# Performance work log

Hardware: AMD Instinct MI355X
Metric: run time of the kernel (lower is better)

The kernel has to match this reference:

```python
import jax, jax.numpy as jnp
import numpy as np

D, L, C, H, W = 4, 16, 64, 128, 128


def setup_inputs() -> dict:
    key = jax.random.key(0)
    ks = jax.random.split(key, 20)
    rn = lambda k, shape, s=0.02: jax.random.normal(k, shape, dtype=jnp.float32) * s
    return {
        "x": jax.random.normal(ks[0], (L, C, H, W), dtype=jnp.float32),
        "ln1_g": jnp.ones((D, C, H, W), jnp.float32),
        "ln1_b": jnp.zeros((D, C, H, W), jnp.float32),
        "Wq": rn(ks[1], (D, C, C)), "bq": jnp.zeros((D, C), jnp.float32),
        "Wk": rn(ks[2], (D, C, C)), "bk": jnp.zeros((D, C), jnp.float32),
        "Wv": rn(ks[3], (D, C, C)), "bv": jnp.zeros((D, C), jnp.float32),
        "Wa": rn(ks[4], (D, 1, 2 * C, 5, 5)), "ba": jnp.zeros((D, 1), jnp.float32),
        "ln2_g": jnp.ones((D, C, H, W), jnp.float32),
        "ln2_b": jnp.zeros((D, C, H, W), jnp.float32),
        "W1": rn(ks[5], (D, 2 * C, C)), "b1": jnp.zeros((D, 2 * C), jnp.float32),
        "W2": rn(ks[6], (D, C, 2 * C)), "b2": jnp.zeros((D, C), jnp.float32),
    }


def _layernorm(x, g, b):
    # torch nn.LayerNorm([C,H,W]): normalize over last 3 dims per frame, eps=1e-5
    mu = jnp.mean(x, axis=(1, 2, 3), keepdims=True)
    var = jnp.var(x, axis=(1, 2, 3), keepdims=True)
    return (x - mu) * jax.lax.rsqrt(var + 1e-5) * g[None] + b[None]


def _conv5(x, w):
    # x: [L, Cin, H, W], w: [1, Cin, 5, 5] -> [L, 1, H, W], SAME padding (pad=2)
    return jax.lax.conv_general_dilated(
        x, w, window_strides=(1, 1), padding="SAME",
        dimension_numbers=("NCHW", "OIHW", "NCHW"))


def _conv1x1(x, w, b):
    # 1x1 conv == per-pixel linear over channels
    return jnp.einsum("lchw,oc->lohw", x, w) + b[None, :, None, None]


def reference(x, ln1_g, ln1_b, Wq, bq, Wk, bk, Wv, bv, Wa, ba,
              ln2_g, ln2_b, W1, b1, W2, b2):
    depth = ln1_g.shape[0]
    c = Wa.shape[2] // 2
    for d in range(depth):
        # --- pre-norm conv attention (nheads=1) + residual ---
        h = _layernorm(x, ln1_g[d], ln1_b[d])
        Q = _conv1x1(h, Wq[d], bq[d])
        K = _conv1x1(h, Wk[d], bk[d])
        V = _conv1x1(h, Wv[d], bv[d])
        # conv_atten(cat([Q_i, K_j])) is linear in channels: split the 5x5
        # kernel into Q-part and K-part, so H_ij = A_i + B_j + bias.
        A = _conv5(Q, Wa[d, :, :c])[:, 0]   # [L, H, W]
        B = _conv5(K, Wa[d, :, c:])[:, 0]   # [L, H, W]
        S = A[:, None] + B[None, :] + ba[d][0]      # [L, L, H, W]
        P = jax.nn.softmax(S, axis=1)               # softmax over source frames j
        attn = jnp.einsum("ijhw,jchw->ichw", P, V)  # weighted sum of V_j
        x = x + attn
        # --- pre-norm conv FFN + residual ---
        h = _layernorm(x, ln2_g[d], ln2_b[d])
        f = _conv1x1(h, W1[d], b1[d])
        f = jax.nn.leaky_relu(f, 0.01)  # torch LeakyReLU default slope
        f = _conv1x1(f, W2[d], b2[d])
        x = x + f
    return x
```

## Files before the change

kernel.cpp:

```cpp
#include <hip/hip_runtime.h>


#define HW 16384
#define CHW 1048576
#define NB 64

typedef unsigned short u16;
typedef __attribute__((ext_vector_type(8))) short bf16x8;
typedef __attribute__((ext_vector_type(8))) unsigned short u16x8;
typedef __attribute__((ext_vector_type(4))) float f32x4;

static __device__ __forceinline__ u16 f2bf(float f) {
  union { float f; unsigned int u; } v; v.f = f;
  unsigned int r = v.u + 0x7fffu + ((v.u >> 16) & 1u);
  return (u16)(r >> 16);
}
static __device__ __forceinline__ float bf2f(u16 h) {
  union { unsigned int u; float f; } v; v.u = ((unsigned int)h) << 16;
  return v.f;
}
static __device__ __forceinline__ void ln_from_acc_wave(
    const float* acc, int l, int lane, float& mu, float& r) {
  const float invN = 1.f / 1048576.f;
  float2 v = *(const float2*)(acc + lane * 32 + 2 * l);
  float s = v.x, q = v.y;
#pragma unroll
  for (int off = 32; off > 0; off >>= 1) {
    s += __shfl_xor(s, off);
    q += __shfl_xor(q, off);
  }
  mu = s * invN;
  r = rsqrtf(q * invN - mu * mu + 1e-5f);
}

__global__ __launch_bounds__(256) void prep_kernel(
    const float* __restrict__ Wa, const float* __restrict__ Wk,
    const float* __restrict__ Wv, const float* __restrict__ W1,
    const float* __restrict__ W2, u16* __restrict__ w1pk,
    u16* __restrict__ w2pk, u16* __restrict__ wvpk, u16* __restrict__ wepk) {
  int d = blockIdx.x;
  int t = blockIdx.y * 256 + threadIdx.x;
  const int STR = 256 * 16;
  const float* WaK = Wa + ((size_t)d * 128 + 64) * 25;
  const float* Wkd = Wk + d * 4096;
  for (int idx = t; idx < 2048; idx += STR) {
    int frag = idx >> 9, lane = (idx >> 3) & 63, j = idx & 7;
    int mt = frag >> 1, kt = frag & 1;
    int tap = mt * 16 + (lane & 15);
    int ci = kt * 32 + (lane >> 4) * 8 + j;
    float s = 0.f;
    if (tap < 25)
      for (int co = 0; co < 64; ++co)
        s = fmaf(WaK[co * 25 + tap], Wkd[co * 64 + ci], s);
    wepk[d * 2048 + idx] = f2bf(s);
  }
  const float* Wvd = Wv + d * 4096;
  for (int idx = t; idx < 4096; idx += STR) {
    int frag = idx >> 9, lane = (idx >> 3) & 63, j = idx & 7;
    int mt = frag >> 1, kt = frag & 1;
    int co = mt * 16 + (lane & 15);
    int ci = kt * 32 + (lane >> 4) * 8 + j;
    wvpk[d * 4096 + idx] = f2bf(Wvd[co * 64 + ci]);
  }
  const float* W1d = W1 + d * 8192;
  for (int idx = t; idx < 8192; idx += STR) {
    int frag = idx >> 9, lane = (idx >> 3) & 63, j = idx & 7;
    int mt = frag >> 1, kt = frag & 1;
    int o = mt * 16 + (lane & 15);
    int ci = kt * 32 + (lane >> 4) * 8 + j;
    w1pk[d * 8192 + idx] = f2bf(W1d[o * 64 + ci]);
  }
  const float* W2d = W2 + d * 8192;
  for (int idx = t; idx < 8192; idx += STR) {
    int frag = idx >> 9, lane = (idx >> 3) & 63, j = idx & 7;
    int mt2 = frag >> 2, kt2 = frag & 3;
    int c = mt2 * 16 + (lane & 15);
    int o = kt2 * 32 + (lane >> 4) * 8 + j;
    w2pk[d * 8192 + idx] = f2bf(W2d[c * 128 + o]);
  }
}

__global__ __launch_bounds__(256) void lngb_kernel(
    const float* __restrict__ g1, const float* __restrict__ b1,
    const float* __restrict__ g2, const float* __restrict__ b2,
    u16* __restrict__ o1, u16* __restrict__ o2, u16* __restrict__ o3,
    u16* __restrict__ o4) {
  int idx = blockIdx.x * 256 + threadIdx.x;
  const float* src;
  u16* dst;
  switch (blockIdx.y) {
    case 0: src = g1; dst = o1; break;
    case 1: src = b1; dst = o2; break;
    case 2: src = g2; dst = o3; break;
    default: src = b2; dst = o4; break;
  }
  float4 v = *(const float4*)(src + (size_t)idx * 4);
  ushort4 o;
  o.x = f2bf(v.x); o.y = f2bf(v.y); o.z = f2bf(v.z); o.w = f2bf(v.w);
  *(ushort4*)(dst + (size_t)idx * 4) = o;
}

__global__ __launch_bounds__(256) void stats_kernel(
    const float* __restrict__ xin, float* __restrict__ acc) {
  int tid = threadIdx.x;
  size_t base = (size_t)blockIdx.x * 4096;
  const float4* in4 = (const float4*)(xin + base);
  float s = 0.f, q = 0.f;
#pragma unroll
  for (int k = 0; k < 4; ++k) {
    float4 v = in4[k * 256 + tid];
    s += v.x + v.y + v.z + v.w;
    q = fmaf(v.x, v.x, q); q = fmaf(v.y, v.y, q);
    q = fmaf(v.z, v.z, q); q = fmaf(v.w, v.w, q);
  }
#pragma unroll
  for (int off = 32; off > 0; off >>= 1) {
    s += __shfl_down(s, off); q += __shfl_down(q, off);
  }
  __shared__ float ls[4], lq[4];
  int wave = tid >> 6;
  if ((tid & 63) == 0) { ls[wave] = s; lq[wave] = q; }
  __syncthreads();
  if (tid == 0) {
    int frame = blockIdx.x >> 8;
    int bkt = blockIdx.x & (NB - 1);
    atomicAdd(&acc[bkt * 32 + frame * 2], ls[0] + ls[1] + ls[2] + ls[3]);
    atomicAdd(&acc[bkt * 32 + frame * 2 + 1], lq[0] + lq[1] + lq[2] + lq[3]);
  }
}

__global__ __launch_bounds__(256) void tb_kernel(
    const float* __restrict__ x, const u16* __restrict__ g,
    const u16* __restrict__ bln, const u16* __restrict__ wep_g,
    const float* __restrict__ accA, float* __restrict__ accBz,
    float* __restrict__ mulr, u16* __restrict__ T) {
  __shared__ __align__(16) char lds[18432];
  u16* hb = (u16*)lds;
  int tid = threadIdx.x;
  int l = blockIdx.y;
  int p0 = blockIdx.x << 7;
  if (blockIdx.x == 0 && blockIdx.y == 0)
    for (int i = tid; i < NB * 32; i += 256) accBz[i] = 0.f;
  int lane = tid & 63;
  float mu, r;
  ln_from_acc_wave(accA, l, lane, mu, r);
  if (blockIdx.x == 0 && tid == 0) {
    mulr[2 * l] = mu;
    mulr[2 * l + 1] = r;
  }

#pragma unroll
  for (int it = 0; it < 2; ++it) {
    int pq = tid & 31, cg = (tid >> 5) + it * 8;
    int px = pq * 4, c0 = cg * 4;
    float vv[4][4];
#pragma unroll
    for (int i = 0; i < 4; ++i) {
      int c = c0 + i;
      size_t gi = (((size_t)l * 64 + c) << 14) + p0 + px;
      int li = (c << 14) + p0 + px;
      float4 xv = *(const float4*)(x + gi);
      ushort4 gv = *(const ushort4*)(g + li);
      ushort4 bb = *(const ushort4*)(bln + li);
      vv[i][0] = (xv.x - mu) * r * bf2f(gv.x) + bf2f(bb.x);
      vv[i][1] = (xv.y - mu) * r * bf2f(gv.y) + bf2f(bb.y);
      vv[i][2] = (xv.z - mu) * r * bf2f(gv.z) + bf2f(bb.z);
      vv[i][3] = (xv.w - mu) * r * bf2f(gv.w) + bf2f(bb.w);
    }
#pragma unroll
    for (int k = 0; k < 4; ++k) {
      int row = px + k;
      int col = ((((c0 >> 3) + (row >> 2)) & 7) << 3) | (c0 & 7);
      ushort4 hv;
      hv.x = f2bf(vv[0][k]); hv.y = f2bf(vv[1][k]);
      hv.z = f2bf(vv[2][k]); hv.w = f2bf(vv[3][k]);
      *(ushort4*)(hb + row * 72 + col) = hv;
    }
  }
  __syncthreads();

  int wv = tid >> 6;
  int ln15 = lane & 15, quad = lane >> 4;

  bf16x8 ah[2][2];
#pragma unroll
  for (int mt = 0; mt < 2; ++mt) {
    int px = (wv * 2 + mt) * 16 + ln15;
#pragma unroll
    for (int kt = 0; kt < 2; ++kt) {
      int slot = ((kt * 4 + quad) + (px >> 2)) & 7;
      ah[mt][kt] = *(const bf16x8*)(hb + px * 72 + (slot << 3));
    }
  }
  const bf16x8* weg = (const bf16x8*)wep_g;

  f32x4 accT[2][2];
#pragma unroll
  for (int mt = 0; mt < 2; ++mt)
#pragma unroll
    for (int nt = 0; nt < 2; ++nt) accT[mt][nt] = (f32x4){0.f, 0.f, 0.f, 0.f};
#pragma unroll
  for (int nt = 0; nt < 2; ++nt) {
    bf16x8 b0 = weg[(nt * 2 + 0) * 64 + lane];
    bf16x8 b1w = weg[(nt * 2 + 1) * 64 + lane];
#pragma unroll
    for (int mt = 0; mt < 2; ++mt) {
      accT[mt][nt] = __builtin_amdgcn_mfma_f32_16x16x32_bf16(
          ah[mt][0], b0, accT[mt][nt], 0, 0, 0);
      accT[mt][nt] = __builtin_amdgcn_mfma_f32_16x16x32_bf16(
          ah[mt][1], b1w, accT[mt][nt], 0, 0, 0);
    }
  }

#pragma unroll
  for (int mt = 0; mt < 2; ++mt) {
    int pxb = p0 + (wv * 2 + mt) * 16 + quad * 4;
#pragma unroll
    for (int nt = 0; nt < 2; ++nt) {
      int tap = nt * 16 + ln15;
      if (tap < 25) {
        ushort4 o;
        o.x = f2bf(accT[mt][nt][0]); o.y = f2bf(accT[mt][nt][1]);
        o.z = f2bf(accT[mt][nt][2]); o.w = f2bf(accT[mt][nt][3]);
        *(ushort4*)(T + (((size_t)l * 25 + tap) << 14) + pxb) = o;
      }
    }
  }
}

__global__ __launch_bounds__(256) void bconv_kernel(
    const u16* __restrict__ T, float* __restrict__ B) {
  int gid = blockIdx.x * 256 + threadIdx.x;
  int l = gid >> 14, p = gid & 16383;
  int y = p >> 7, xx = p & 127;
  float s = 0.f;
#pragma unroll
  for (int dy = 0; dy < 5; ++dy) {
    int yy = y + dy - 2;
    if (yy < 0 || yy > 127) continue;
#pragma unroll
    for (int dx = 0; dx < 5; ++dx) {
      int xc = xx + dx - 2;
      if (xc < 0 || xc > 127) continue;
      s += bf2f(T[(((size_t)l * 25 + dy * 5 + dx) << 14) + (yy << 7) + xc]);
    }
  }
  B[gid] = s;
}

__global__ __launch_bounds__(256) void attnc_kernel(
    const float* __restrict__ x, const float* __restrict__ B,
    const u16* __restrict__ g1, const u16* __restrict__ b1g,
    const u16* __restrict__ wvp_g, const float* __restrict__ bv,
    const float* __restrict__ mulr, u16* __restrict__ abf,
    float* __restrict__ accB, float* __restrict__ accAz) {
  __shared__ float Prl[16][64];
  __shared__ float scal[64];
  __shared__ __align__(16) u16 hb[64 * 72];
  __shared__ float lsq[4][32];
  int tid = threadIdx.x;
  int p0 = blockIdx.x << 6;
  if (blockIdx.x == 0)
    for (int i = tid; i < NB * 32; i += 256) accAz[i] = 0.f;

  if (tid < 64) {
    float bj[16], m = -1e30f;
#pragma unroll
    for (int j = 0; j < 16; ++j) {
      bj[j] = B[(j << 14) + p0 + tid];
      m = fmaxf(m, bj[j]);
    }
    float sum = 0.f;
#pragma unroll
    for (int j = 0; j < 16; ++j) {
      bj[j] = __expf(bj[j] - m);
      sum += bj[j];
    }
    float inv = 1.f / sum;
    float sc = 0.f;
#pragma unroll
    for (int j = 0; j < 16; ++j) {
      float mu_j = mulr[2 * j], r_j = mulr[2 * j + 1];
      float prl = bj[j] * inv * r_j;
      Prl[j][tid] = prl;
      sc = fmaf(prl, mu_j, sc);
    }
    scal[tid] = sc;
  }
  __syncthreads();

  int csub = tid >> 4, pxq = tid & 15;
  f32x4 xbar[4];
#pragma unroll
  for (int cc = 0; cc < 4; ++cc) xbar[cc] = (f32x4){0.f, 0.f, 0.f, 0.f};
#pragma unroll
  for (int j = 0; j < 16; ++j) {
    f32x4 P4 = *(const f32x4*)&Prl[j][pxq * 4];
#pragma unroll
    for (int cc = 0; cc < 4; ++cc) {
      int c = cc * 16 + csub;
      float4 xv =
          *(const float4*)(x + (((size_t)j * 64 + c) << 14) + p0 + pxq * 4);
      xbar[cc][0] = fmaf(P4[0], xv.x, xbar[cc][0]);
      xbar[cc][1] = fmaf(P4[1], xv.y, xbar[cc][1]);
      xbar[cc][2] = fmaf(P4[2], xv.z, xbar[cc][2]);
      xbar[cc][3] = fmaf(P4[3], xv.w, xbar[cc][3]);
    }
  }
  {
    f32x4 sc4 = *(const f32x4*)&scal[pxq * 4];
#pragma unroll
    for (int cc = 0; cc < 4; ++cc) {
      int c = cc * 16 + csub;
      ushort4 g4 = *(const ushort4*)(g1 + ((size_t)c << 14) + p0 + pxq * 4);
      ushort4 b4 = *(const ushort4*)(b1g + ((size_t)c << 14) + p0 + pxq * 4);
      float hv[4];
      hv[0] = bf2f(g4.x) * (xbar[cc][0] - sc4[0]) + bf2f(b4.x);
      hv[1] = bf2f(g4.y) * (xbar[cc][1] - sc4[1]) + bf2f(b4.y);
      hv[2] = bf2f(g4.z) * (xbar[cc][2] - sc4[2]) + bf2f(b4.z);
      hv[3] = bf2f(g4.w) * (xbar[cc][3] - sc4[3]) + bf2f(b4.w);
#pragma unroll
      for (int k = 0; k < 4; ++k) {
        int row = pxq * 4 + k;
        int col = ((((c >> 3) + (row >> 2)) & 7) << 3) | (c & 7);
        hb[row * 72 + col] = f2bf(hv[k]);
      }
    }
  }
  __syncthreads();

  int wv = tid >> 6, lane = tid & 63;
  int ln15 = lane & 15, quad = lane >> 4;
  int px = wv * 16 + ln15;
  bf16x8 ah[2];
#pragma unroll
  for (int kt = 0; kt < 2; ++kt) {
    int slot = ((kt * 4 + quad) + (px >> 2)) & 7;
    ah[kt] = *(const bf16x8*)(hb + px * 72 + (slot << 3));
  }
  const bf16x8* wvg = (const bf16x8*)wvp_g;
  f32x4 accV[4];
#pragma unroll
  for (int nt = 0; nt < 4; ++nt) accV[nt] = (f32x4){0.f, 0.f, 0.f, 0.f};
#pragma unroll
  for (int nt = 0; nt < 4; ++nt) {
    bf16x8 b0 = wvg[(nt * 2 + 0) * 64 + lane];
    bf16x8 b1w = wvg[(nt * 2 + 1) * 64 + lane];
    accV[nt] = __builtin_amdgcn_mfma_f32_16x16x32_bf16(ah[0], b0, accV[nt],
                                                       0, 0, 0);
    accV[nt] = __builtin_amdgcn_mfma_f32_16x16x32_bf16(ah[1], b1w, accV[nt],
                                                       0, 0, 0);
  }
  int pxb = p0 + wv * 16 + quad * 4;
  float av[4][4];
#pragma unroll
  for (int nt = 0; nt < 4; ++nt) {
    int c = nt * 16 + ln15;
    float bvc = bv[c];
    ushort4 o;
    av[nt][0] = accV[nt][0] + bvc; o.x = f2bf(av[nt][0]);
    av[nt][1] = accV[nt][1] + bvc; o.y = f2bf(av[nt][1]);
    av[nt][2] = accV[nt][2] + bvc; o.z = f2bf(av[nt][2]);
    av[nt][3] = accV[nt][3] + bvc; o.w = f2bf(av[nt][3]);
    *(ushort4*)(abf + ((size_t)c << 14) + pxb) = o;
  }

  float sf[16], qf[16];
#pragma unroll
  for (int f = 0; f < 16; ++f) {
    float s = 0.f, q = 0.f;
#pragma unroll
    for (int nt = 0; nt < 4; ++nt) {
      int c = nt * 16 + ln15;
      float4 xv =
          *(const float4*)(x + ((size_t)f << 20) + ((size_t)c << 14) + pxb);
      float v0 = xv.x + av[nt][0], v1 = xv.y + av[nt][1];
      float v2 = xv.z + av[nt][2], v3 = xv.w + av[nt][3];
      s += v0 + v1 + v2 + v3;
      q = fmaf(v0, v0, q); q = fmaf(v1, v1, q);
      q = fmaf(v2, v2, q); q = fmaf(v3, v3, q);
    }
    sf[f] = s; qf[f] = q;
  }
#pragma unroll
  for (int off = 32; off > 0; off >>= 1) {
#pragma unroll
    for (int f = 0; f < 16; ++f) {
      sf[f] += __shfl_down(sf[f], off);
      qf[f] += __shfl_down(qf[f], off);
    }
  }
  if (lane == 0) {
#pragma unroll
    for (int f = 0; f < 16; ++f) {
      lsq[wv][2 * f] = sf[f];
      lsq[wv][2 * f + 1] = qf[f];
    }
  }
  __syncthreads();
  if (tid < 32) {
    int bkt = blockIdx.x & (NB - 1);
    atomicAdd(&accB[bkt * 32 + tid],
              lsq[0][tid] + lsq[1][tid] + lsq[2][tid] + lsq[3][tid]);
  }
}

__global__ __launch_bounds__(256) void ffn_kernel(
    const float* __restrict__ xr, float* __restrict__ xw,
    const u16* __restrict__ ap, const u16* __restrict__ g,
    const u16* __restrict__ bln, const u16* __restrict__ w1p_g,
    const float* __restrict__ b1, const u16* __restrict__ w2p_g,
    const float* __restrict__ b2, const float* __restrict__ accB,
    float* __restrict__ accA) {
  __shared__ __align__(16) char lds[66560];
  float* xaf = (float*)lds;
  u16* hb = (u16*)(lds + 33792);
  u16* f1 = (u16*)(lds + 33792);

  int tid = threadIdx.x;
  int P0 = blockIdx.x << 7;
  int l = P0 >> 14;
  int p0 = P0 & 16383;
  int lane = tid & 63;
  float mu, r;
  ln_from_acc_wave(accB, l, lane, mu, r);

#pragma unroll
  for (int it = 0; it < 2; ++it) {
    int pq = tid & 31, cg = (tid >> 5) + it * 8;
    int px = pq * 4, c0 = cg * 4;
    float vv[4][4];
#pragma unroll
    for (int i = 0; i < 4; ++i) {
      int c = c0 + i;
      size_t gi = (((size_t)l * 64 + c) << 14) + p0 + px;
      int li = (c << 14) + p0 + px;
      float4 xv = *(const float4*)(xr + gi);
      ushort4 av4 = *(const ushort4*)(ap + li);
      ushort4 gv = *(const ushort4*)(g + li);
      ushort4 bb = *(const ushort4*)(bln + li);
      float4 s4;
      s4.x = xv.x + bf2f(av4.x); s4.y = xv.y + bf2f(av4.y);
      s4.z = xv.z + bf2f(av4.z); s4.w = xv.w + bf2f(av4.w);
      *(float4*)(xaf + c * 132 + px) = s4;
      vv[i][0] = (s4.x - mu) * r * bf2f(gv.x) + bf2f(bb.x);
      vv[i][1] = (s4.y - mu) * r * bf2f(gv.y) + bf2f(bb.y);
      vv[i][2] = (s4.z - mu) * r * bf2f(gv.z) + bf2f(bb.z);
      vv[i][3] = (s4.w - mu) * r * bf2f(gv.w) + bf2f(bb.w);
    }
#pragma unroll
    for (int k = 0; k < 4; ++k) {
      int row = px + k;
      int col = ((((c0 >> 3) + (row >> 2)) & 7) << 3) | (c0 & 7);
      ushort4 hv;
      hv.x = f2bf(vv[0][k]); hv.y = f2bf(vv[1][k]);
      hv.z = f2bf(vv[2][k]); hv.w = f2bf(vv[3][k]);
      *(ushort4*)(hb + row * 72 + col) = hv;
    }
  }
  __syncthreads();

  int wv = tid >> 6;
  int ln15 = lane & 15, quad = lane >> 4;

  bf16x8 bh[2][2];
#pragma unroll
  for (int nt = 0; nt < 2; ++nt) {
    int px = (wv * 2 + nt) * 16 + ln15;
#pragma unroll
    for (int kt = 0; kt < 2; ++kt) {
      int slot = ((kt * 4 + quad) + (px >> 2)) & 7;
      bh[nt][kt] = *(const bf16x8*)(hb + px * 72 + (slot << 3));
    }
  }
  __syncthreads();

  const bf16x8* w1g = (const bf16x8*)w1p_g;
  const bf16x8* w2g = (const bf16x8*)w2p_g;

#pragma unroll
  for (int mt = 0; mt < 8; ++mt) {
    bf16x8 a1a = w1g[(mt * 2 + 0) * 64 + lane];
    bf16x8 a1b = w1g[(mt * 2 + 1) * 64 + lane];
    f32x4 acc[2];
    acc[0] = (f32x4){0.f, 0.f, 0.f, 0.f};
    acc[1] = (f32x4){0.f, 0.f, 0.f, 0.f};
#pragma unroll
    for (int nt = 0; nt < 2; ++nt) {
      acc[nt] = __builtin_amdgcn_mfma_f32_16x16x32_bf16(a1a, bh[nt][0],
                                                        acc[nt], 0, 0, 0);
      acc[nt] = __builtin_amdgcn_mfma_f32_16x16x32_bf16(a1b, bh[nt][1],
                                                        acc[nt], 0, 0, 0);
    }
    int o0 = mt * 16 + quad * 4;
    float4 b1v = *(const float4*)(b1 + o0);
#pragma unroll
    for (int nt = 0; nt < 2; ++nt) {
      int px = (wv * 2 + nt) * 16 + ln15;
      int swz = (px & 7) * 8;
      float fv[4];
#pragma unroll
      for (int rj = 0; rj < 4; ++rj) {
        float f = acc[nt][rj] + ((const float*)&b1v)[rj];
        fv[rj] = fmaxf(f, 0.01f * f);
      }
      int col = ((o0 & ~7) ^ swz) + (o0 & 7);
      ushort4 ov;
      ov.x = f2bf(fv[0]); ov.y = f2bf(fv[1]);
      ov.z = f2bf(fv[2]); ov.w = f2bf(fv[3]);
      *(ushort4*)(f1 + px * 128 + col) = ov;
    }
  }
  __syncthreads();

  bf16x8 a2[2][4];
#pragma unroll
  for (int mt = 0; mt < 2; ++mt) {
    int px = (wv * 2 + mt) * 16 + ln15;
    int swz = (px & 7) * 8;
#pragma unroll
    for (int kt = 0; kt < 4; ++kt)
      a2[mt][kt] =
          *(const bf16x8*)(f1 + px * 128 + ((kt * 32 + quad * 8) ^ swz));
  }
  f32x4 acc2[2][4];
#pragma unroll
  for (int mt = 0; mt < 2; ++mt)
#pragma unroll
    for (int nt = 0; nt < 4; ++nt) acc2[mt][nt] = (f32x4){0.f, 0.f, 0.f, 0.f};
#pragma unroll
  for (int nt = 0; nt < 4; ++nt) {
    bf16x8 bw[4];
#pragma unroll
    for (int kt = 0; kt < 4; ++kt) bw[kt] = w2g[(nt * 4 + kt) * 64 + lane];
#pragma unroll
    for (int mt = 0; mt < 2; ++mt)
#pragma unroll
      for (int kt = 0; kt < 4; ++kt)
        acc2[mt][nt] = __builtin_amdgcn_mfma_f32_16x16x32_bf16(
            a2[mt][kt], bw[kt], acc2[mt][nt], 0, 0, 0);
  }

  float s = 0.f, q = 0.f;
#pragma unroll
  for (int mt = 0; mt < 2; ++mt) {
    int pxl = (wv * 2 + mt) * 16 + quad * 4;
#pragma unroll
    for (int nt = 0; nt < 4; ++nt) {
      int c = nt * 16 + ln15;
      float b2c = b2[c];
      const float* xac = xaf + c * 132 + pxl;
      float4 v;
      v.x = xac[0] + acc2[mt][nt][0] + b2c;
      v.y = xac[1] + acc2[mt][nt][1] + b2c;
      v.z = xac[2] + acc2[mt][nt][2] + b2c;
      v.w = xac[3] + acc2[mt][nt][3] + b2c;
      *(float4*)(xw + (((size_t)l * 64 + c) << 14) + p0 + pxl) = v;
      s += v.x + v.y + v.z + v.w;
      q = fmaf(v.x, v.x, q); q = fmaf(v.y, v.y, q);
      q = fmaf(v.z, v.z, q); q = fmaf(v.w, v.w, q);
    }
  }
#pragma unroll
  for (int off = 32; off > 0; off >>= 1) {
    s += __shfl_down(s, off); q += __shfl_down(q, off);
  }
  if (lane == 0) {
    int bkt = blockIdx.x & (NB - 1);
    atomicAdd(&accA[bkt * 32 + l * 2], s);
    atomicAdd(&accA[bkt * 32 + l * 2 + 1], q);
  }
}

extern "C" void kernel_launch(void* const* d_in, const int* in_sizes, int n_in,
                              void* d_out, int out_size, void* d_ws,
                              size_t ws_size, hipStream_t stream) {
  const float* x_in = (const float*)d_in[0];
  const float* ln1_g = (const float*)d_in[1];
  const float* ln1_b = (const float*)d_in[2];
  const float* Wk = (const float*)d_in[5];
  const float* Wv = (const float*)d_in[7];
  const float* bv = (const float*)d_in[8];
  const float* Wa = (const float*)d_in[9];
  const float* ln2_g = (const float*)d_in[11];
  const float* ln2_b = (const float*)d_in[12];
  const float* W1 = (const float*)d_in[13];
  const float* b1 = (const float*)d_in[14];
  const float* W2 = (const float*)d_in[15];
  const float* b2 = (const float*)d_in[16];

  float* xbuf = (float*)d_out;
  char* wsb = (char*)d_ws;
  u16* T = (u16*)wsb;
  u16* abf = (u16*)(wsb + 13107200);
  float* Bbuf = (float*)(wsb + 15204352);
  u16* g1b = (u16*)(wsb + 16252928);
  u16* b1bb = (u16*)(wsb + 24641536);
  u16* g2b = (u16*)(wsb + 33030144);
  u16* b2bb = (u16*)(wsb + 41418752);
  u16* w1pk = (u16*)(wsb + 49807360);
  u16* w2pk = (u16*)(wsb + 49872896);
  u16* wvpk = (u16*)(wsb + 49938432);
  u16* wepk = (u16*)(wsb + 49971200);
  float* mulr = (float*)(wsb + 49987584);
  float* accA = (float*)(wsb + 49987712);
  float* accB = (float*)(wsb + 49995904);

  hipMemsetAsync(accA, 0, 16384, stream);
  prep_kernel<<<dim3(4, 16), 256, 0, stream>>>(Wa, Wk, Wv, W1, W2, w1pk, w2pk,
                                               wvpk, wepk);
  lngb_kernel<<<dim3(4096, 4), 256, 0, stream>>>(ln1_g, ln1_b, ln2_g, ln2_b,
                                                 g1b, b1bb, g2b, b2bb);
  stats_kernel<<<4096, 256, 0, stream>>>(x_in, accA);

  const float* xr = x_in;
  for (int d = 0; d < 4; ++d) {
    tb_kernel<<<dim3(128, 16), 256, 0, stream>>>(
        xr, g1b + (size_t)d * CHW, b1bb + (size_t)d * CHW, wepk + d * 2048,
        accA, accB, mulr, T);
    bconv_kernel<<<1024, 256, 0, stream>>>(T, Bbuf);
    attnc_kernel<<<256, 256, 0, stream>>>(
        xr, Bbuf, g1b + (size_t)d * CHW, b1bb + (size_t)d * CHW,
        wvpk + d * 4096, bv + d * 64, mulr, abf, accB, accA);
    ffn_kernel<<<2048, 256, 0, stream>>>(
        xr, xbuf, abf, g2b + (size_t)d * CHW, b2bb + (size_t)d * CHW,
        w1pk + d * 8192, b1 + d * 128, w2pk + d * 8192, b2 + d * 64, accB,
        accA);
    xr = xbuf;
  }
}
```

Measured before the change: 565.2 us.

## Keep a bf16 shadow copy of x for attention reads and drop LN-param conversions

The stats and FFN kernels now also write a bf16 copy of the residual stream x, and the tb and attnc kernels read that copy instead of fp32 x, halving bytes on their heaviest reads. The bf16 conversion of ln1_b, ln2_g and ln2_b is removed; those kernels read the fp32 originals, shrinking the one-time preprocessing pass. tb and attnc also switch to 8-wide vector loads per thread. The trade is extra bf16 write traffic from the FFN and stats kernels, more fp32 bytes for some LN parameters, and lower precision on the x values used in attention.

Measured after the change: 561.6 us. About the same (-0.6%).

```diff
diff --git a/kernel.cpp b/kernel.cpp
--- a/kernel.cpp
+++ b/kernel.cpp
@@ -81,27 +81,17 @@
 }
 
 __global__ __launch_bounds__(256) void lngb_kernel(
-    const float* __restrict__ g1, const float* __restrict__ b1,
-    const float* __restrict__ g2, const float* __restrict__ b2,
-    u16* __restrict__ o1, u16* __restrict__ o2, u16* __restrict__ o3,
-    u16* __restrict__ o4) {
+    const float* __restrict__ g1, u16* __restrict__ o1) {
   int idx = blockIdx.x * 256 + threadIdx.x;
-  const float* src;
-  u16* dst;
-  switch (blockIdx.y) {
-    case 0: src = g1; dst = o1; break;
-    case 1: src = b1; dst = o2; break;
-    case 2: src = g2; dst = o3; break;
-    default: src = b2; dst = o4; break;
-  }
-  float4 v = *(const float4*)(src + (size_t)idx * 4);
+  float4 v = *(const float4*)(g1 + (size_t)idx * 4);
   ushort4 o;
   o.x = f2bf(v.x); o.y = f2bf(v.y); o.z = f2bf(v.z); o.w = f2bf(v.w);
-  *(ushort4*)(dst + (size_t)idx * 4) = o;
+  *(ushort4*)(o1 + (size_t)idx * 4) = o;
 }
 
 __global__ __launch_bounds__(256) void stats_kernel(
-    const float* __restrict__ xin, float* __restrict__ acc) {
+    const float* __restrict__ xin, u16* __restrict__ xbf,
+    float* __restrict__ acc) {
   int tid = threadIdx.x;
   size_t base = (size_t)blockIdx.x * 4096;
   const float4* in4 = (const float4*)(xin + base);
@@ -109,6 +99,9 @@
 #pragma unroll
   for (int k = 0; k < 4; ++k) {
     float4 v = in4[k * 256 + tid];
+    ushort4 o;
+    o.x = f2bf(v.x); o.y = f2bf(v.y); o.z = f2bf(v.z); o.w = f2bf(v.w);
+    *(ushort4*)(xbf + base + (k * 256 + tid) * 4) = o;
     s += v.x + v.y + v.z + v.w;
     q = fmaf(v.x, v.x, q); q = fmaf(v.y, v.y, q);
     q = fmaf(v.z, v.z, q); q = fmaf(v.w, v.w, q);
@@ -130,8 +123,8 @@
 }
 
 __global__ __launch_bounds__(256) void tb_kernel(
-    const float* __restrict__ x, const u16* __restrict__ g,
-    const u16* __restrict__ bln, const u16* __restrict__ wep_g,
+    const u16* __restrict__ xbf, const u16* __restrict__ g,
+    const float* __restrict__ bln, const u16* __restrict__ wep_g,
     const float* __restrict__ accA, float* __restrict__ accBz,
     float* __restrict__ mulr, u16* __restrict__ T) {
   __shared__ __align__(16) char lds[18432];
@@ -149,27 +142,28 @@
     mulr[2 * l + 1] = r;
   }
 
-#pragma unroll
-  for (int it = 0; it < 2; ++it) {
-    int pq = tid & 31, cg = (tid >> 5) + it * 8;
-    int px = pq * 4, c0 = cg * 4;
-    float vv[4][4];
+  {
+    int pq = tid & 15, cg = tid >> 4;
+    int px0 = pq * 8, c0 = cg * 4;
+    float vv[4][8];
 #pragma unroll
     for (int i = 0; i < 4; ++i) {
       int c = c0 + i;
-      size_t gi = (((size_t)l * 64 + c) << 14) + p0 + px;
-      int li = (c << 14) + p0 + px;
-      float4 xv = *(const float4*)(x + gi);
-      ushort4 gv = *(const ushort4*)(g + li);
-      ushort4 bb = *(const ushort4*)(bln + li);
-      vv[i][0] = (xv.x - mu) * r * bf2f(gv.x) + bf2f(bb.x);
-      vv[i][1] = (xv.y - mu) * r * bf2f(gv.y) + bf2f(bb.y);
-      vv[i][2] = (xv.z - mu) * r * bf2f(gv.z) + bf2f(bb.z);
-      vv[i][3] = (xv.w - mu) * r * bf2f(gv.w) + bf2f(bb.w);
-    }
-#pragma unroll
-    for (int k = 0; k < 4; ++k) {
-      int row = px + k;
+      size_t gi = (((size_t)l * 64 + c) << 14) + p0 + px0;
+      int li = (c << 14) + p0 + px0;
+      u16x8 xv = *(const u16x8*)(xbf + gi);
+      u16x8 gv = *(const u16x8*)(g + li);
+      float4 bb0 = *(const float4*)(bln + li);
+      float4 bb1 = *(const float4*)(bln + li + 4);
+#pragma unroll
+      for (int k = 0; k < 8; ++k) {
+        float bbk = k < 4 ? ((const float*)&bb0)[k] : ((const float*)&bb1)[k - 4];
+        vv[i][k] = (bf2f(xv[k]) - mu) * r * bf2f(gv[k]) + bbk;
+      }
+    }
+#pragma unroll
+    for (int k = 0; k < 8; ++k) {
+      int row = px0 + k;
       int col = ((((c0 >> 3) + (row >> 2)) & 7) << 3) | (c0 & 7);
       ushort4 hv;
       hv.x = f2bf(vv[0][k]); hv.y = f2bf(vv[1][k]);
@@ -249,8 +243,8 @@
 }
 
 __global__ __launch_bounds__(256) void attnc_kernel(
-    const float* __restrict__ x, const float* __restrict__ B,
-    const u16* __restrict__ g1, const u16* __restrict__ b1g,
+    const u16* __restrict__ xbf, const float* __restrict__ B,
+    const u16* __restrict__ g1, const float* __restrict__ b1g,
     const u16* __restrict__ wvp_g, const float* __restrict__ bv,
     const float* __restrict__ mulr, u16* __restrict__ abf,
     float* __restrict__ accB, float* __restrict__ accAz) {
@@ -289,41 +283,46 @@
   }
   __syncthreads();
 
-  int csub = tid >> 4, pxq = tid & 15;
-  f32x4 xbar[4];
-#pragma unroll
-  for (int cc = 0; cc < 4; ++cc) xbar[cc] = (f32x4){0.f, 0.f, 0.f, 0.f};
-#pragma unroll
-  for (int j = 0; j < 16; ++j) {
-    f32x4 P4 = *(const f32x4*)&Prl[j][pxq * 4];
-#pragma unroll
-    for (int cc = 0; cc < 4; ++cc) {
-      int c = cc * 16 + csub;
-      float4 xv =
-          *(const float4*)(x + (((size_t)j * 64 + c) << 14) + p0 + pxq * 4);
-      xbar[cc][0] = fmaf(P4[0], xv.x, xbar[cc][0]);
-      xbar[cc][1] = fmaf(P4[1], xv.y, xbar[cc][1]);
-      xbar[cc][2] = fmaf(P4[2], xv.z, xbar[cc][2]);
-      xbar[cc][3] = fmaf(P4[3], xv.w, xbar[cc][3]);
-    }
-  }
   {
-    f32x4 sc4 = *(const f32x4*)&scal[pxq * 4];
-#pragma unroll
-    for (int cc = 0; cc < 4; ++cc) {
-      int c = cc * 16 + csub;
-      ushort4 g4 = *(const ushort4*)(g1 + ((size_t)c << 14) + p0 + pxq * 4);
-      ushort4 b4 = *(const ushort4*)(b1g + ((size_t)c << 14) + p0 + pxq * 4);
-      float hv[4];
-      hv[0] = bf2f(g4.x) * (xbar[cc][0] - sc4[0]) + bf2f(b4.x);
-      hv[1] = bf2f(g4.y) * (xbar[cc][1] - sc4[1]) + bf2f(b4.y);
-      hv[2] = bf2f(g4.z) * (xbar[cc][2] - sc4[2]) + bf2f(b4.z);
-      hv[3] = bf2f(g4.w) * (xbar[cc][3] - sc4[3]) + bf2f(b4.w);
-#pragma unroll
-      for (int k = 0; k < 4; ++k) {
-        int row = pxq * 4 + k;
+    int c2 = tid >> 3, pxg = tid & 7;
+    int px0 = pxg * 8;
+    float xbar[2][8];
+#pragma unroll
+    for (int cc = 0; cc < 2; ++cc)
+#pragma unroll
+      for (int k = 0; k < 8; ++k) xbar[cc][k] = 0.f;
+#pragma unroll
+    for (int j = 0; j < 16; ++j) {
+      float p8[8];
+#pragma unroll
+      for (int k = 0; k < 8; ++k) p8[k] = Prl[j][px0 + k];
+#pragma unroll
+      for (int cc = 0; cc < 2; ++cc) {
+        int c = cc * 32 + c2;
+        u16x8 xv =
+            *(const u16x8*)(xbf + (((size_t)j * 64 + c) << 14) + p0 + px0);
+#pragma unroll
+        for (int k = 0; k < 8; ++k)
+          xbar[cc][k] = fmaf(p8[k], bf2f(xv[k]), xbar[cc][k]);
+      }
+    }
+    float sc8[8];
+#pragma unroll
+    for (int k = 0; k < 8; ++k) sc8[k] = scal[px0 + k];
+#pragma unroll
+    for (int cc = 0; cc < 2; ++cc) {
+      int c = cc * 32 + c2;
+      int li = (c << 14) + p0 + px0;
+      u16x8 g8 = *(const u16x8*)(g1 + li);
+      float4 b0 = *(const float4*)(b1g + li);
+      float4 b1v = *(const float4*)(b1g + li + 4);
+#pragma unroll
+      for (int k = 0; k < 8; ++k) {
+        float bbk = k < 4 ? ((const float*)&b0)[k] : ((const float*)&b1v)[k - 4];
+        float hv = bf2f(g8[k]) * (xbar[cc][k] - sc8[k]) + bbk;
+        int row = px0 + k;
         int col = ((((c >> 3) + (row >> 2)) & 7) << 3) | (c & 7);
-        hb[row * 72 + col] = f2bf(hv[k]);
+        hb[row * 72 + col] = f2bf(hv);
       }
     }
   }
@@ -372,10 +371,10 @@
 #pragma unroll
     for (int nt = 0; nt < 4; ++nt) {
       int c = nt * 16 + ln15;
-      float4 xv =
-          *(const float4*)(x + ((size_t)f << 20) + ((size_t)c << 14) + pxb);
-      float v0 = xv.x + av[nt][0], v1 = xv.y + av[nt][1];
-      float v2 = xv.z + av[nt][2], v3 = xv.w + av[nt][3];
+      ushort4 xv =
+          *(const ushort4*)(xbf + (((size_t)f * 64 + c) << 14) + pxb);
+      float v0 = bf2f(xv.x) + av[nt][0], v1 = bf2f(xv.y) + av[nt][1];
+      float v2 = bf2f(xv.z) + av[nt][2], v3 = bf2f(xv.w) + av[nt][3];
       s += v0 + v1 + v2 + v3;
       q = fmaf(v0, v0, q); q = fmaf(v1, v1, q);
       q = fmaf(v2, v2, q); q = fmaf(v3, v3, q);
@@ -407,11 +406,11 @@
 
 __global__ __launch_bounds__(256) void ffn_kernel(
     const float* __restrict__ xr, float* __restrict__ xw,
-    const u16* __restrict__ ap, const u16* __restrict__ g,
-    const u16* __restrict__ bln, const u16* __restrict__ w1p_g,
-    const float* __restrict__ b1, const u16* __restrict__ w2p_g,
-    const float* __restrict__ b2, const float* __restrict__ accB,
-    float* __restrict__ accA) {
+    u16* __restrict__ xbfw, const u16* __restrict__ ap,
+    const float* __restrict__ g, const float* __restrict__ bln,
+    const u16* __restrict__ w1p_g, const float* __restrict__ b1,
+    const u16* __restrict__ w2p_g, const float* __restrict__ b2,
+    const float* __restrict__ accB, float* __restrict__ accA, int wrbf) {
   __shared__ __align__(16) char lds[66560];
   float* xaf = (float*)lds;
   u16* hb = (u16*)(lds + 33792);
@@ -437,16 +436,16 @@
       int li = (c << 14) + p0 + px;
       float4 xv = *(const float4*)(xr + gi);
       ushort4 av4 = *(const ushort4*)(ap + li);
-      ushort4 gv = *(const ushort4*)(g + li);
-      ushort4 bb = *(const ushort4*)(bln + li);
+      float4 gv = *(const float4*)(g + li);
+      float4 bb = *(const float4*)(bln + li);
       float4 s4;
       s4.x = xv.x + bf2f(av4.x); s4.y = xv.y + bf2f(av4.y);
       s4.z = xv.z + bf2f(av4.z); s4.w = xv.w + bf2f(av4.w);
       *(float4*)(xaf + c * 132 + px) = s4;
-      vv[i][0] = (s4.x - mu) * r * bf2f(gv.x) + bf2f(bb.x);
-      vv[i][1] = (s4.y - mu) * r * bf2f(gv.y) + bf2f(bb.y);
-      vv[i][2] = (s4.z - mu) * r * bf2f(gv.z) + bf2f(bb.z);
-      vv[i][3] = (s4.w - mu) * r * bf2f(gv.w) + bf2f(bb.w);
+      vv[i][0] = (s4.x - mu) * r * gv.x + bb.x;
+      vv[i][1] = (s4.y - mu) * r * gv.y + bb.y;
+      vv[i][2] = (s4.z - mu) * r * gv.z + bb.z;
+      vv[i][3] = (s4.w - mu) * r * gv.w + bb.w;
     }
 #pragma unroll
     for (int k = 0; k < 4; ++k) {
@@ -555,7 +554,13 @@
       v.y = xac[1] + acc2[mt][nt][1] + b2c;
       v.z = xac[2] + acc2[mt][nt][2] + b2c;
       v.w = xac[3] + acc2[mt][nt][3] + b2c;
-      *(float4*)(xw + (((size_t)l * 64 + c) << 14) + p0 + pxl) = v;
+      size_t gi = (((size_t)l * 64 + c) << 14) + p0 + pxl;
+      *(float4*)(xw + gi) = v;
+      if (wrbf) {
+        ushort4 o;
+        o.x = f2bf(v.x); o.y = f2bf(v.y); o.z = f2bf(v.z); o.w = f2bf(v.w);
+        *(ushort4*)(xbfw + gi) = o;
+      }
       s += v.x + v.y + v.z + v.w;
       q = fmaf(v.x, v.x, q); q = fmaf(v.y, v.y, q);
       q = fmaf(v.z, v.z, q); q = fmaf(v.w, v.w, q);
@@ -591,41 +596,38 @@
 
   float* xbuf = (float*)d_out;
   char* wsb = (char*)d_ws;
-  u16* T = (u16*)wsb;
-  u16* abf = (u16*)(wsb + 13107200);
-  float* Bbuf = (float*)(wsb + 15204352);
-  u16* g1b = (u16*)(wsb + 16252928);
-  u16* b1bb = (u16*)(wsb + 24641536);
-  u16* g2b = (u16*)(wsb + 33030144);
-  u16* b2bb = (u16*)(wsb + 41418752);
-  u16* w1pk = (u16*)(wsb + 49807360);
-  u16* w2pk = (u16*)(wsb + 49872896);
-  u16* wvpk = (u16*)(wsb + 49938432);
-  u16* wepk = (u16*)(wsb + 49971200);
-  float* mulr = (float*)(wsb + 49987584);
-  float* accA = (float*)(wsb + 49987712);
-  float* accB = (float*)(wsb + 49995904);
+  u16* xbf = (u16*)wsb;
+  u16* T = (u16*)(wsb + 33554432);
+  u16* abf = (u16*)(wsb + 46661632);
+  float* Bbuf = (float*)(wsb + 48758784);
+  u16* g1b = (u16*)(wsb + 49807360);
+  u16* w1pk = (u16*)(wsb + 58195968);
+  u16* w2pk = (u16*)(wsb + 58261504);
+  u16* wvpk = (u16*)(wsb + 58327040);
+  u16* wepk = (u16*)(wsb + 58359808);
+  float* mulr = (float*)(wsb + 58376192);
+  float* accA = (float*)(wsb + 58376320);
+  float* accB = (float*)(wsb + 58384512);
 
   hipMemsetAsync(accA, 0, 16384, stream);
   prep_kernel<<<dim3(4, 16), 256, 0, stream>>>(Wa, Wk, Wv, W1, W2, w1pk, w2pk,
                                                wvpk, wepk);
-  lngb_kernel<<<dim3(4096, 4), 256, 0, stream>>>(ln1_g, ln1_b, ln2_g, ln2_b,
-                                                 g1b, b1bb, g2b, b2bb);
-  stats_kernel<<<4096, 256, 0, stream>>>(x_in, accA);
+  lngb_kernel<<<4096, 256, 0, stream>>>(ln1_g, g1b);
+  stats_kernel<<<4096, 256, 0, stream>>>(x_in, xbf, accA);
 
   const float* xr = x_in;
   for (int d = 0; d < 4; ++d) {
     tb_kernel<<<dim3(128, 16), 256, 0, stream>>>(
-        xr, g1b + (size_t)d * CHW, b1bb + (size_t)d * CHW, wepk + d * 2048,
+        xbf, g1b + (size_t)d * CHW, ln1_b + (size_t)d * CHW, wepk + d * 2048,
         accA, accB, mulr, T);
     bconv_kernel<<<1024, 256, 0, stream>>>(T, Bbuf);
     attnc_kernel<<<256, 256, 0, stream>>>(
-        xr, Bbuf, g1b + (size_t)d * CHW, b1bb + (size_t)d * CHW,
+        xbf, Bbuf, g1b + (size_t)d * CHW, ln1_b + (size_t)d * CHW,
         wvpk + d * 4096, bv + d * 64, mulr, abf, accB, accA);
     ffn_kernel<<<2048, 256, 0, stream>>>(
-        xr, xbuf, abf, g2b + (size_t)d * CHW, b2bb + (size_t)d * CHW,
+        xr, xbuf, xbf, abf, ln2_g + (size_t)d * CHW, ln2_b + (size_t)d * CHW,
         w1pk + d * 8192, b1 + d * 128, w2pk + d * 8192, b2 + d * 64, accB,
-        accA);
+        accA, d < 3 ? 1 : 0);
     xr = xbuf;
   }
 }
```
